# Kernel tuning notes

Hardware: AMD Instinct MI355X
Metric: run time of the kernel (lower is better)

## Reference

```python
import jax, jax.numpy as jnp
import numpy as np

B, S, D_MODEL, H = 2, 2048, 1024, 16
DH = D_MODEL // H  # head size = 64
NEG = -1e12


def setup_inputs() -> dict:
    key = jax.random.key(0)
    ks = jax.random.split(key, 10)
    x = jax.random.normal(ks[0], (B, S, D_MODEL), dtype=jnp.float32)
    # realistic padding mask: random valid lengths in [S//2, S]
    lengths = jax.random.randint(ks[1], (B,), S // 2, S + 1)
    mask = jnp.arange(S)[None, :] < lengths[:, None]  # [B, S] bool
    init = 0.02
    Wq = jax.random.normal(ks[2], (D_MODEL, D_MODEL), jnp.float32) * init
    Wk = jax.random.normal(ks[3], (D_MODEL, D_MODEL), jnp.float32) * init
    Wv = jax.random.normal(ks[4], (D_MODEL, D_MODEL), jnp.float32) * init
    Wr = jax.random.normal(ks[5], (D_MODEL, D_MODEL), jnp.float32) * init
    bq = jnp.zeros((D_MODEL,), jnp.float32)
    bk = jnp.zeros((D_MODEL,), jnp.float32)
    bv = jnp.zeros((D_MODEL,), jnp.float32)
    br = jnp.zeros((D_MODEL,), jnp.float32)
    return {"x": x, "mask": mask, "Wq": Wq, "bq": bq, "Wk": Wk, "bk": bk,
            "Wv": Wv, "bv": bv, "Wr": Wr, "br": br}


def reference(x, mask, Wq, bq, Wk, bk, Wv, bv, Wr, br):
    # x: [B,S,D]; mask: [B,S] bool (True = valid token)
    def heads(w, b):
        y = x @ w + b                         # [B,S,D]
        return y.reshape(B, S, H, DH).transpose(0, 2, 1, 3)  # [B,H,S,DH]

    qw, kw, vw = heads(Wq, bq), heads(Wk, bk), heads(Wv, bv)
    scores = jnp.einsum('bhqd,bhkd->bhqk', qw, kw) / jnp.sqrt(jnp.float32(DH))
    # padding mask on key axis ('-inf' fill)
    scores = jnp.where(mask[:, None, None, :], scores, NEG)
    # lm (causal, lower-triangular) additive mask
    causal = jnp.tril(jnp.ones((S, S), dtype=bool))
    scores = scores + jnp.where(causal, 0.0, NEG)[None, None]
    a = jax.nn.softmax(scores, axis=-1)
    o = jnp.einsum('bhqk,bhkd->bhqd', a, vw)          # [B,H,S,DH]
    o = o.transpose(0, 2, 1, 3).reshape(B, S, D_MODEL)  # [B,S,D]
    # second padding mask on output (value=0, sequence axis)
    o = o * mask[:, :, None].astype(o.dtype)
    # residual projection
    o = o + (x @ Wr + br)
    return o
```

## Files before the change

kernel.cpp:

```cpp
#include <hip/hip_runtime.h>
#include <hip/hip_bf16.h>

#define BQ 2
#define SEQ 2048
#define DM 1024
#define NH 16
#define DHEAD 64

typedef unsigned short u16;
typedef unsigned int u32;
typedef __attribute__((ext_vector_type(8))) short short8;
typedef __attribute__((ext_vector_type(4))) float f32x4;

__device__ __forceinline__ u16 f2b(float f) {
    unsigned u = __builtin_bit_cast(unsigned, f);
    unsigned r = u + 0x7fffu + ((u >> 16) & 1u);
    return (u16)(r >> 16);
}

__device__ __forceinline__ void gld_lds16(const void* g, void* l) {
    __builtin_amdgcn_global_load_lds(
        (const __attribute__((address_space(1))) void*)g,
        (__attribute__((address_space(3))) void*)l, 16, 0, 0);
}


__global__ __launch_bounds__(256) void cvt_x_kernel(const float* __restrict__ x,
                                                    u16* __restrict__ xb) {
    int i = blockIdx.x * 256 + threadIdx.x;
    float4 v = ((const float4*)x)[i];
    ushort4 o;
    o.x = f2b(v.x); o.y = f2b(v.y); o.z = f2b(v.z); o.w = f2b(v.w);
    ((ushort4*)xb)[i] = o;
}

__global__ __launch_bounds__(256) void pack_w4(
        const float* __restrict__ W0, const float* __restrict__ W1,
        const float* __restrict__ W2, const float* __restrict__ W3,
        u16* __restrict__ wt) {
    __shared__ u16 Ws[64][68];
    const float* W = (blockIdx.z == 0) ? W0 : (blockIdx.z == 1) ? W1
                   : (blockIdx.z == 2) ? W2 : W3;
    const int k0 = blockIdx.x * 64, d0 = blockIdx.y * 64;
    const int t = threadIdx.x;
    const int lrow = t >> 4, lcol = (t & 15) * 4;
    #pragma unroll
    for (int i = 0; i < 4; i++) {
        float4 v = *(const float4*)(W + (size_t)(k0 + lrow + i * 16) * DM + d0 + lcol);
        Ws[lrow + i * 16][lcol + 0] = f2b(v.x);
        Ws[lrow + i * 16][lcol + 1] = f2b(v.y);
        Ws[lrow + i * 16][lcol + 2] = f2b(v.z);
        Ws[lrow + i * 16][lcol + 3] = f2b(v.w);
    }
    __syncthreads();
    const int dl = t >> 2, kq = (t & 3) * 16;
    uint4 o1, o2;
    o1.x = (u32)Ws[kq + 0][dl]  | ((u32)Ws[kq + 1][dl]  << 16);
    o1.y = (u32)Ws[kq + 2][dl]  | ((u32)Ws[kq + 3][dl]  << 16);
    o1.z = (u32)Ws[kq + 4][dl]  | ((u32)Ws[kq + 5][dl]  << 16);
    o1.w = (u32)Ws[kq + 6][dl]  | ((u32)Ws[kq + 7][dl]  << 16);
    o2.x = (u32)Ws[kq + 8][dl]  | ((u32)Ws[kq + 9][dl]  << 16);
    o2.y = (u32)Ws[kq + 10][dl] | ((u32)Ws[kq + 11][dl] << 16);
    o2.z = (u32)Ws[kq + 12][dl] | ((u32)Ws[kq + 13][dl] << 16);
    o2.w = (u32)Ws[kq + 14][dl] | ((u32)Ws[kq + 15][dl] << 16);
    u16* dst = wt + (size_t)(blockIdx.z * DM + d0 + dl) * DM + k0 + kq;
    *(uint4*)(dst) = o1;
    *(uint4*)(dst + 8) = o2;
}

__global__ __launch_bounds__(256) void pack_bias_kernel(const float* __restrict__ b0,
                                                        const float* __restrict__ b1,
                                                        const float* __restrict__ b2,
                                                        const float* __restrict__ b3,
                                                        float* __restrict__ bias) {
    int i = blockIdx.x * 256 + threadIdx.x;
    const float* s = (i < 1024) ? b0 : (i < 2048) ? b1 : (i < 3072) ? b2 : b3;
    bias[i] = s[i & 1023];
}

__global__ __launch_bounds__(256) void calc_len_kernel(const int* __restrict__ mask,
                                                       int* __restrict__ lengths) {
    __shared__ int cnt[BQ];
    if (threadIdx.x < BQ) cnt[threadIdx.x] = 0;
    __syncthreads();
    for (int b = 0; b < BQ; b++) {
        int c = 0;
        for (int s = threadIdx.x; s < SEQ; s += 256)
            c += (mask[b * SEQ + s] != 0) ? 1 : 0;
        atomicAdd(&cnt[b], c);
    }
    __syncthreads();
    if (threadIdx.x < BQ) lengths[threadIdx.x] = cnt[threadIdx.x];
}


__global__ __launch_bounds__(256) void gemm_qkvr(
        const u16* __restrict__ xb, const u16* __restrict__ wt,
        const float* __restrict__ bias,
        u16* __restrict__ qbuf, u16* __restrict__ kbuf, u16* __restrict__ vbuf,
        float* __restrict__ out) {
    __shared__ __align__(16) u16 As[128 * 32];
    __shared__ __align__(16) u16 Bs[128 * 32];
    const int tid = threadIdx.x;
    const int wid = tid >> 6, lane = tid & 63;
    const int lr = lane & 15, lg = lane >> 4;
    const int bm = blockIdx.x, bn = blockIdx.y;
    const int wm = (wid >> 1) * 64, wn = (wid & 1) * 64;

    const int crow = lane >> 2, ccol = (lane & 3) * 8;
    const u16* agp0 = xb + (size_t)(bm * 128 + (wid * 2 + 0) * 16 + crow) * DM + ccol;
    const u16* agp1 = xb + (size_t)(bm * 128 + (wid * 2 + 1) * 16 + crow) * DM + ccol;
    const u16* bgp0 = wt + (size_t)(bn * 128 + (wid * 2 + 0) * 16 + crow) * DM + ccol;
    const u16* bgp1 = wt + (size_t)(bn * 128 + (wid * 2 + 1) * 16 + crow) * DM + ccol;
    u16* al0 = As + (wid * 2 + 0) * 512;
    u16* al1 = As + (wid * 2 + 1) * 512;
    u16* bl0 = Bs + (wid * 2 + 0) * 512;
    u16* bl1 = Bs + (wid * 2 + 1) * 512;

    f32x4 acc[4][4] = {};

    for (int kk = 0; kk < DM; kk += 32) {
        gld_lds16(agp0 + kk, al0);
        gld_lds16(agp1 + kk, al1);
        gld_lds16(bgp0 + kk, bl0);
        gld_lds16(bgp1 + kk, bl1);
        __syncthreads();
        short8 af[4], bfr[4];
        #pragma unroll
        for (int mt = 0; mt < 4; mt++)
            af[mt] = *(const short8*)(As + (wm + mt * 16 + lr) * 32 + lg * 8);
        #pragma unroll
        for (int nt = 0; nt < 4; nt++)
            bfr[nt] = *(const short8*)(Bs + (wn + nt * 16 + lr) * 32 + lg * 8);
        #pragma unroll
        for (int mt = 0; mt < 4; mt++)
            #pragma unroll
            for (int nt = 0; nt < 4; nt++)
                acc[mt][nt] = __builtin_amdgcn_mfma_f32_16x16x32_bf16(
                        af[mt], bfr[nt], acc[mt][nt], 0, 0, 0);
        __syncthreads();
    }

    #pragma unroll
    for (int nt = 0; nt < 4; nt++) {
        int n = bn * 128 + wn + nt * 16 + lr;
        int which = n >> 10, d = n & 1023;
        float bv_ = bias[n];
        #pragma unroll
        for (int mt = 0; mt < 4; mt++) {
            #pragma unroll
            for (int r = 0; r < 4; r++) {
                int m = bm * 128 + wm + mt * 16 + lg * 4 + r;
                float y = acc[mt][nt][r] + bv_;
                if (which == 3) {
                    out[(size_t)m * DM + d] = y;
                } else {
                    int h = d >> 6, dh = d & 63;
                    int b = m >> 11, s = m & (SEQ - 1);
                    size_t idx = ((size_t)(b * NH + h) * SEQ + s) * DHEAD + dh;
                    u16 hv = f2b(y);
                    if (which == 0) qbuf[idx] = hv;
                    else if (which == 1) kbuf[idx] = hv;
                    else vbuf[idx] = hv;
                }
            }
        }
    }
}


__global__ __launch_bounds__(256) void attn_kernel(
        const u16* __restrict__ qbuf, const u16* __restrict__ kbuf,
        const u16* __restrict__ vbuf, const int* __restrict__ lengths,
        float* __restrict__ out) {
    __shared__ __align__(16) u32 Vt[64 * 32];
    __shared__ __align__(16) u32 Pl[4][32 * 32];

    const int qt = blockIdx.x, bh = blockIdx.y;
    const int b = bh >> 4, h = bh & 15;
    const int len = lengths[b];
    const int qbase = qt * 128;
    if (qbase >= len) return;

    const int tid = threadIdx.x, wid = tid >> 6, lane = tid & 63;
    const int lr = lane & 15, lg = lane >> 4;
    const int qw = qbase + wid * 32;
    const int swz = (lr & 7) << 2;

    const u16* qp = qbuf + (size_t)bh * SEQ * DHEAD;
    const u16* kp = kbuf + (size_t)bh * SEQ * DHEAD;
    const u16* vp = vbuf + (size_t)bh * SEQ * DHEAD;

    short8 bq[2][2];
    #pragma unroll
    for (int ntq = 0; ntq < 2; ntq++)
        #pragma unroll
        for (int ks = 0; ks < 2; ks++)
            bq[ntq][ks] = *(const short8*)(qp + (size_t)(qw + ntq * 16 + lr) * DHEAD + ks * 32 + lg * 8);

    f32x4 oacc[4][2] = {};
    float mrow[2] = {-3.0e38f, -3.0e38f};
    float lsum[2] = {0.0f, 0.0f};

    const int nkt = 2 * qt + 2;
    const int vk = (tid & 31) * 2, vd = (tid >> 5) * 8;

    for (int kt = 0; kt < nkt; kt++) {
        const int kbase = kt * 64;
        const bool active  = (kbase <= qw + 31);
        const bool maskful = (kbase + 63 > qw);

        const u16* vrow = vp + (size_t)(kbase + vk) * DHEAD + vd;
        uint4 va = *(const uint4*)vrow;
        uint4 vb2 = *(const uint4*)(vrow + DHEAD);

        f32x4 sc[4][2] = {};
        float scl[2] = {1.0f, 1.0f};
        if (active) {
            #pragma unroll
            for (int mtk = 0; mtk < 4; mtk++) {
                #pragma unroll
                for (int ks = 0; ks < 2; ks++) {
                    short8 ak = *(const short8*)(kp + (size_t)(kbase + mtk * 16 + lr) * DHEAD + ks * 32 + lg * 8);
                    #pragma unroll
                    for (int ntq = 0; ntq < 2; ntq++)
                        sc[mtk][ntq] = __builtin_amdgcn_mfma_f32_16x16x32_bf16(
                                ak, bq[ntq][ks], sc[mtk][ntq], 0, 0, 0);
                }
            }
            if (maskful) {
                #pragma unroll
                for (int mtk = 0; mtk < 4; mtk++) {
                    int keyb = kbase + mtk * 16 + lg * 4;
                    #pragma unroll
                    for (int ntq = 0; ntq < 2; ntq++) {
                        int qq = qw + ntq * 16 + lr;
                        #pragma unroll
                        for (int r = 0; r < 4; r++)
                            sc[mtk][ntq][r] = (keyb + r > qq) ? -3.0e38f
                                                              : sc[mtk][ntq][r] * 0.125f;
                    }
                }
            } else {
                #pragma unroll
                for (int mtk = 0; mtk < 4; mtk++)
                    #pragma unroll
                    for (int ntq = 0; ntq < 2; ntq++)
                        #pragma unroll
                        for (int r = 0; r < 4; r++)
                            sc[mtk][ntq][r] *= 0.125f;
            }
            #pragma unroll
            for (int ntq = 0; ntq < 2; ntq++) {
                float mx = sc[0][ntq][0];
                #pragma unroll
                for (int mtk = 0; mtk < 4; mtk++)
                    #pragma unroll
                    for (int r = 0; r < 4; r++)
                        mx = fmaxf(mx, sc[mtk][ntq][r]);
                mx = fmaxf(mx, __shfl_xor(mx, 16, 64));
                mx = fmaxf(mx, __shfl_xor(mx, 32, 64));
                float mnew = fmaxf(mrow[ntq], mx);
                float sq = __expf(mrow[ntq] - mnew);
                mrow[ntq] = mnew;
                float ps = 0.0f;
                #pragma unroll
                for (int mtk = 0; mtk < 4; mtk++)
                    #pragma unroll
                    for (int r = 0; r < 4; r++) {
                        float p = __expf(sc[mtk][ntq][r] - mnew);
                        sc[mtk][ntq][r] = p;
                        ps += p;
                    }
                ps += __shfl_xor(ps, 16, 64);
                ps += __shfl_xor(ps, 32, 64);
                lsum[ntq] = lsum[ntq] * sq + ps;
                scl[ntq] = sq;
            }
            #pragma unroll
            for (int mtd = 0; mtd < 4; mtd++)
                #pragma unroll
                for (int ntq = 0; ntq < 2; ntq++)
                    #pragma unroll
                    for (int r = 0; r < 4; r++)
                        oacc[mtd][ntq][r] *= scl[ntq];
        }

        __syncthreads();

        {
            union { uint4 v; u16 s[8]; } ua, ub;
            ua.v = va; ub.v = vb2;
            #pragma unroll
            for (int j = 0; j < 8; j++) {
                u32 w = (u32)ua.s[j] | ((u32)ub.s[j] << 16);
                Vt[(vd + j) * 32 + ((tid & 31) ^ (j << 2))] = w;
            }
        }
        if (active) {
            #pragma unroll
            for (int ntq = 0; ntq < 2; ntq++) {
                int rowbase = (ntq * 16 + lr) * 32;
                #pragma unroll
                for (int mtk = 0; mtk < 4; mtk++)
                    #pragma unroll
                    for (int i = 0; i < 2; i++) {
                        u32 w = (u32)f2b(sc[mtk][ntq][2 * i])
                              | ((u32)f2b(sc[mtk][ntq][2 * i + 1]) << 16);
                        Pl[wid][rowbase + ((mtk * 8 + lg * 2 + i) ^ swz)] = w;
                    }
            }
        }

        __syncthreads();

        if (active) {
            #pragma unroll
            for (int ks = 0; ks < 2; ks++) {
                int wv = (ks * 16 + lg * 4) ^ swz;
                short8 bp0 = *(const short8*)&Pl[wid][(lr) * 32 + wv];
                short8 bp1 = *(const short8*)&Pl[wid][(16 + lr) * 32 + wv];
                #pragma unroll
                for (int mtd = 0; mtd < 4; mtd++) {
                    short8 av = *(const short8*)&Vt[(mtd * 16 + lr) * 32 + wv];
                    oacc[mtd][0] = __builtin_amdgcn_mfma_f32_16x16x32_bf16(av, bp0, oacc[mtd][0], 0, 0, 0);
                    oacc[mtd][1] = __builtin_amdgcn_mfma_f32_16x16x32_bf16(av, bp1, oacc[mtd][1], 0, 0, 0);
                }
            }
        }
    }

    #pragma unroll
    for (int ntq = 0; ntq < 2; ntq++) {
        int q = qw + ntq * 16 + lr;
        if (q < len) {
            float inv = 1.0f / lsum[ntq];
            float* orow = out + (size_t)(b * SEQ + q) * DM + h * DHEAD;
            #pragma unroll
            for (int mtd = 0; mtd < 4; mtd++)
                #pragma unroll
                for (int r = 0; r < 4; r++)
                    orow[mtd * 16 + lg * 4 + r] += oacc[mtd][ntq][r] * inv;
        }
    }
}


extern "C" void kernel_launch(void* const* d_in, const int* in_sizes, int n_in,
                              void* d_out, int out_size, void* d_ws, size_t ws_size,
                              hipStream_t stream) {
    const float* x  = (const float*)d_in[0];
    const int*  mask = (const int*)d_in[1];
    const float* Wq = (const float*)d_in[2];
    const float* bq = (const float*)d_in[3];
    const float* Wk = (const float*)d_in[4];
    const float* bk = (const float*)d_in[5];
    const float* Wv = (const float*)d_in[6];
    const float* bv = (const float*)d_in[7];
    const float* Wr = (const float*)d_in[8];
    const float* br = (const float*)d_in[9];
    float* out = (float*)d_out;

    char* ws = (char*)d_ws;
    size_t off = 0;
    auto alloc = [&](size_t bytes) {
        size_t o = off; off = (off + bytes + 255) & ~(size_t)255; return o;
    };
    u16* xb   = (u16*)(ws + alloc((size_t)BQ * SEQ * DM * 2));
    u16* wt   = (u16*)(ws + alloc((size_t)4 * DM * DM * 2));
    float* bias = (float*)(ws + alloc(4 * DM * 4));
    u16* qbuf = (u16*)(ws + alloc((size_t)BQ * NH * SEQ * DHEAD * 2));
    u16* kbuf = (u16*)(ws + alloc((size_t)BQ * NH * SEQ * DHEAD * 2));
    u16* vbuf = (u16*)(ws + alloc((size_t)BQ * NH * SEQ * DHEAD * 2));
    int* lens = (int*)(ws + alloc(256));

    hipLaunchKernelGGL(cvt_x_kernel, dim3((BQ * SEQ * DM) / 4 / 256), dim3(256), 0, stream, x, xb);
    hipLaunchKernelGGL(pack_w4, dim3(16, 16, 4), dim3(256), 0, stream, Wq, Wk, Wv, Wr, wt);
    hipLaunchKernelGGL(pack_bias_kernel, dim3(16), dim3(256), 0, stream, bq, bk, bv, br, bias);
    hipLaunchKernelGGL(calc_len_kernel, dim3(1), dim3(256), 0, stream, mask, lens);
    hipLaunchKernelGGL(gemm_qkvr, dim3(32, 32), dim3(256), 0, stream,
                       xb, wt, bias, qbuf, kbuf, vbuf, out);
    hipLaunchKernelGGL(attn_kernel, dim3(SEQ / 128, BQ * NH), dim3(256), 0, stream,
                       qbuf, kbuf, vbuf, lens, out);
}
```

Baseline: 172.0 us.

## Split attention into single-wave blocks with reversed scheduling and register-prefetched V

Each attention block becomes one 64-thread wave handling 32 queries, so the per-tile __syncthreads barriers go away and each wave iterates only over the key tiles its causal range needs. The grid is reordered so the heaviest query tiles launch first, for better load balance. The next V tile is prefetched into registers while the current one is used, and softmax switches to exp2 with the log2e factor folded into the scale. In exchange there are four times as many blocks and more register pressure from the 8 uint4 V prefetch registers, with no intra-block sharing of K/V loads.

```diff
diff --git a/kernel.cpp b/kernel.cpp
--- a/kernel.cpp
+++ b/kernel.cpp
@@ -169,22 +169,23 @@
 }
 
 
-__global__ __launch_bounds__(256) void attn_kernel(
+__global__ __launch_bounds__(64, 3) void attn_kernel(
         const u16* __restrict__ qbuf, const u16* __restrict__ kbuf,
         const u16* __restrict__ vbuf, const int* __restrict__ lengths,
         float* __restrict__ out) {
     __shared__ __align__(16) u32 Vt[64 * 32];
-    __shared__ __align__(16) u32 Pl[4][32 * 32];
-
-    const int qt = blockIdx.x, bh = blockIdx.y;
+    __shared__ __align__(16) u32 Pl[32 * 32];
+
+    const int bh = blockIdx.x;
+    const int slice = blockIdx.y;
+    const int qt = (int)gridDim.z - 1 - (int)blockIdx.z;
     const int b = bh >> 4, h = bh & 15;
     const int len = lengths[b];
-    const int qbase = qt * 128;
-    if (qbase >= len) return;
-
-    const int tid = threadIdx.x, wid = tid >> 6, lane = tid & 63;
+    const int qw = qt * 128 + slice * 32;
+    if (qw >= len) return;
+
+    const int lane = threadIdx.x;
     const int lr = lane & 15, lg = lane >> 4;
-    const int qw = qbase + wid * 32;
     const int swz = (lr & 7) << 2;
 
     const u16* qp = qbuf + (size_t)bh * SEQ * DHEAD;
@@ -202,130 +203,141 @@
     float mrow[2] = {-3.0e38f, -3.0e38f};
     float lsum[2] = {0.0f, 0.0f};
 
-    const int nkt = 2 * qt + 2;
-    const int vk = (tid & 31) * 2, vd = (tid >> 5) * 8;
+    const int nkt = (qw >> 6) + 1;
+    const int vk = (lane & 31) * 2;
+    const int vd0 = (lane >> 5) * 8;
+    const float SC = 0.125f * 1.44269504f;
+
+    uint4 vreg[8];
+    #pragma unroll
+    for (int c = 0; c < 4; c++) {
+        const u16* vrow = vp + (size_t)vk * DHEAD + vd0 + c * 16;
+        vreg[2 * c]     = *(const uint4*)vrow;
+        vreg[2 * c + 1] = *(const uint4*)(vrow + DHEAD);
+    }
 
     for (int kt = 0; kt < nkt; kt++) {
         const int kbase = kt * 64;
-        const bool active  = (kbase <= qw + 31);
+
+        #pragma unroll
+        for (int c = 0; c < 4; c++) {
+            union { uint4 v; u16 s[8]; } ua, ub;
+            ua.v = vreg[2 * c]; ub.v = vreg[2 * c + 1];
+            int d = vd0 + c * 16;
+            #pragma unroll
+            for (int j = 0; j < 8; j++) {
+                u32 w = (u32)ua.s[j] | ((u32)ub.s[j] << 16);
+                Vt[(d + j) * 32 + ((vk >> 1) ^ (j << 2))] = w;
+            }
+        }
+        if (kt + 1 < nkt) {
+            #pragma unroll
+            for (int c = 0; c < 4; c++) {
+                const u16* vrow = vp + (size_t)(kbase + 64 + vk) * DHEAD + vd0 + c * 16;
+                vreg[2 * c]     = *(const uint4*)vrow;
+                vreg[2 * c + 1] = *(const uint4*)(vrow + DHEAD);
+            }
+        }
+
+        short8 ak[4][2];
+        #pragma unroll
+        for (int mtk = 0; mtk < 4; mtk++)
+            #pragma unroll
+            for (int ks = 0; ks < 2; ks++)
+                ak[mtk][ks] = *(const short8*)(kp + (size_t)(kbase + mtk * 16 + lr) * DHEAD + ks * 32 + lg * 8);
+        f32x4 sc[4][2] = {};
+        #pragma unroll
+        for (int mtk = 0; mtk < 4; mtk++)
+            #pragma unroll
+            for (int ks = 0; ks < 2; ks++)
+                #pragma unroll
+                for (int ntq = 0; ntq < 2; ntq++)
+                    sc[mtk][ntq] = __builtin_amdgcn_mfma_f32_16x16x32_bf16(
+                            ak[mtk][ks], bq[ntq][ks], sc[mtk][ntq], 0, 0, 0);
+
         const bool maskful = (kbase + 63 > qw);
-
-        const u16* vrow = vp + (size_t)(kbase + vk) * DHEAD + vd;
-        uint4 va = *(const uint4*)vrow;
-        uint4 vb2 = *(const uint4*)(vrow + DHEAD);
-
-        f32x4 sc[4][2] = {};
-        float scl[2] = {1.0f, 1.0f};
-        if (active) {
+        if (maskful) {
             #pragma unroll
             for (int mtk = 0; mtk < 4; mtk++) {
-                #pragma unroll
-                for (int ks = 0; ks < 2; ks++) {
-                    short8 ak = *(const short8*)(kp + (size_t)(kbase + mtk * 16 + lr) * DHEAD + ks * 32 + lg * 8);
-                    #pragma unroll
-                    for (int ntq = 0; ntq < 2; ntq++)
-                        sc[mtk][ntq] = __builtin_amdgcn_mfma_f32_16x16x32_bf16(
-                                ak, bq[ntq][ks], sc[mtk][ntq], 0, 0, 0);
-                }
-            }
-            if (maskful) {
-                #pragma unroll
-                for (int mtk = 0; mtk < 4; mtk++) {
-                    int keyb = kbase + mtk * 16 + lg * 4;
-                    #pragma unroll
-                    for (int ntq = 0; ntq < 2; ntq++) {
-                        int qq = qw + ntq * 16 + lr;
-                        #pragma unroll
-                        for (int r = 0; r < 4; r++)
-                            sc[mtk][ntq][r] = (keyb + r > qq) ? -3.0e38f
-                                                              : sc[mtk][ntq][r] * 0.125f;
-                    }
-                }
-            } else {
-                #pragma unroll
-                for (int mtk = 0; mtk < 4; mtk++)
-                    #pragma unroll
-                    for (int ntq = 0; ntq < 2; ntq++)
-                        #pragma unroll
-                        for (int r = 0; r < 4; r++)
-                            sc[mtk][ntq][r] *= 0.125f;
-            }
-            #pragma unroll
-            for (int ntq = 0; ntq < 2; ntq++) {
-                float mx = sc[0][ntq][0];
-                #pragma unroll
-                for (int mtk = 0; mtk < 4; mtk++)
+                int keyb = kbase + mtk * 16 + lg * 4;
+                #pragma unroll
+                for (int ntq = 0; ntq < 2; ntq++) {
+                    int qq = qw + ntq * 16 + lr;
                     #pragma unroll
                     for (int r = 0; r < 4; r++)
-                        mx = fmaxf(mx, sc[mtk][ntq][r]);
-                mx = fmaxf(mx, __shfl_xor(mx, 16, 64));
-                mx = fmaxf(mx, __shfl_xor(mx, 32, 64));
-                float mnew = fmaxf(mrow[ntq], mx);
-                float sq = __expf(mrow[ntq] - mnew);
-                mrow[ntq] = mnew;
-                float ps = 0.0f;
-                #pragma unroll
-                for (int mtk = 0; mtk < 4; mtk++)
-                    #pragma unroll
-                    for (int r = 0; r < 4; r++) {
-                        float p = __expf(sc[mtk][ntq][r] - mnew);
-                        sc[mtk][ntq][r] = p;
-                        ps += p;
-                    }
-                ps += __shfl_xor(ps, 16, 64);
-                ps += __shfl_xor(ps, 32, 64);
-                lsum[ntq] = lsum[ntq] * sq + ps;
-                scl[ntq] = sq;
-            }
-            #pragma unroll
-            for (int mtd = 0; mtd < 4; mtd++)
+                        sc[mtk][ntq][r] = (keyb + r > qq) ? -3.0e38f
+                                                          : sc[mtk][ntq][r] * SC;
+                }
+            }
+        } else {
+            #pragma unroll
+            for (int mtk = 0; mtk < 4; mtk++)
                 #pragma unroll
                 for (int ntq = 0; ntq < 2; ntq++)
                     #pragma unroll
                     for (int r = 0; r < 4; r++)
-                        oacc[mtd][ntq][r] *= scl[ntq];
-        }
-
-        __syncthreads();
-
-        {
-            union { uint4 v; u16 s[8]; } ua, ub;
-            ua.v = va; ub.v = vb2;
-            #pragma unroll
-            for (int j = 0; j < 8; j++) {
-                u32 w = (u32)ua.s[j] | ((u32)ub.s[j] << 16);
-                Vt[(vd + j) * 32 + ((tid & 31) ^ (j << 2))] = w;
-            }
-        }
-        if (active) {
-            #pragma unroll
-            for (int ntq = 0; ntq < 2; ntq++) {
-                int rowbase = (ntq * 16 + lr) * 32;
-                #pragma unroll
-                for (int mtk = 0; mtk < 4; mtk++)
-                    #pragma unroll
-                    for (int i = 0; i < 2; i++) {
-                        u32 w = (u32)f2b(sc[mtk][ntq][2 * i])
-                              | ((u32)f2b(sc[mtk][ntq][2 * i + 1]) << 16);
-                        Pl[wid][rowbase + ((mtk * 8 + lg * 2 + i) ^ swz)] = w;
-                    }
-            }
-        }
-
-        __syncthreads();
-
-        if (active) {
-            #pragma unroll
-            for (int ks = 0; ks < 2; ks++) {
-                int wv = (ks * 16 + lg * 4) ^ swz;
-                short8 bp0 = *(const short8*)&Pl[wid][(lr) * 32 + wv];
-                short8 bp1 = *(const short8*)&Pl[wid][(16 + lr) * 32 + wv];
-                #pragma unroll
-                for (int mtd = 0; mtd < 4; mtd++) {
-                    short8 av = *(const short8*)&Vt[(mtd * 16 + lr) * 32 + wv];
-                    oacc[mtd][0] = __builtin_amdgcn_mfma_f32_16x16x32_bf16(av, bp0, oacc[mtd][0], 0, 0, 0);
-                    oacc[mtd][1] = __builtin_amdgcn_mfma_f32_16x16x32_bf16(av, bp1, oacc[mtd][1], 0, 0, 0);
+                        sc[mtk][ntq][r] *= SC;
+        }
+
+        float scl[2];
+        #pragma unroll
+        for (int ntq = 0; ntq < 2; ntq++) {
+            float mx = sc[0][ntq][0];
+            #pragma unroll
+            for (int mtk = 0; mtk < 4; mtk++)
+                #pragma unroll
+                for (int r = 0; r < 4; r++)
+                    mx = fmaxf(mx, sc[mtk][ntq][r]);
+            mx = fmaxf(mx, __shfl_xor(mx, 16, 64));
+            mx = fmaxf(mx, __shfl_xor(mx, 32, 64));
+            float mnew = fmaxf(mrow[ntq], mx);
+            float sq = exp2f(mrow[ntq] - mnew);
+            mrow[ntq] = mnew;
+            float ps = 0.0f;
+            #pragma unroll
+            for (int mtk = 0; mtk < 4; mtk++)
+                #pragma unroll
+                for (int r = 0; r < 4; r++) {
+                    float p = exp2f(sc[mtk][ntq][r] - mnew);
+                    sc[mtk][ntq][r] = p;
+                    ps += p;
                 }
+            ps += __shfl_xor(ps, 16, 64);
+            ps += __shfl_xor(ps, 32, 64);
+            lsum[ntq] = lsum[ntq] * sq + ps;
+            scl[ntq] = sq;
+        }
+        #pragma unroll
+        for (int mtd = 0; mtd < 4; mtd++)
+            #pragma unroll
+            for (int ntq = 0; ntq < 2; ntq++)
+                #pragma unroll
+                for (int r = 0; r < 4; r++)
+                    oacc[mtd][ntq][r] *= scl[ntq];
+
+        #pragma unroll
+        for (int ntq = 0; ntq < 2; ntq++) {
+            int rowbase = (ntq * 16 + lr) * 32;
+            #pragma unroll
+            for (int mtk = 0; mtk < 4; mtk++)
+                #pragma unroll
+                for (int i = 0; i < 2; i++) {
+                    u32 w = (u32)f2b(sc[mtk][ntq][2 * i])
+                          | ((u32)f2b(sc[mtk][ntq][2 * i + 1]) << 16);
+                    Pl[rowbase + ((mtk * 8 + lg * 2 + i) ^ swz)] = w;
+                }
+        }
+
+        #pragma unroll
+        for (int ks = 0; ks < 2; ks++) {
+            int wv = (ks * 16 + lg * 4) ^ swz;
+            short8 bp0 = *(const short8*)&Pl[(lr) * 32 + wv];
+            short8 bp1 = *(const short8*)&Pl[(16 + lr) * 32 + wv];
+            #pragma unroll
+            for (int mtd = 0; mtd < 4; mtd++) {
+                short8 av = *(const short8*)&Vt[(mtd * 16 + lr) * 32 + wv];
+                oacc[mtd][0] = __builtin_amdgcn_mfma_f32_16x16x32_bf16(av, bp0, oacc[mtd][0], 0, 0, 0);
+                oacc[mtd][1] = __builtin_amdgcn_mfma_f32_16x16x32_bf16(av, bp1, oacc[mtd][1], 0, 0, 0);
             }
         }
     }
@@ -380,6 +392,6 @@
     hipLaunchKernelGGL(calc_len_kernel, dim3(1), dim3(256), 0, stream, mask, lens);
     hipLaunchKernelGGL(gemm_qkvr, dim3(32, 32), dim3(256), 0, stream,
                        xb, wt, bias, qbuf, kbuf, vbuf, out);
-    hipLaunchKernelGGL(attn_kernel, dim3(SEQ / 128, BQ * NH), dim3(256), 0, stream,
+    hipLaunchKernelGGL(attn_kernel, dim3(BQ * NH, 4, SEQ / 128), dim3(64), 0, stream,
                        qbuf, kbuf, vbuf, lens, out);
 }
```

After: 226.9 us. +32.0%, slower.
